# Kernel tuning notes

Measured on AMD Instinct MI355X. Metric: run time of the kernel, lower is better.

The kernel has to match this reference:

```python
import jax, jax.numpy as jnp
import numpy as np

BS, NCAMS, CIN, H, W = 4, 1, 256, 56, 200
MID = 128
DCH = 112  # (58-2)/0.5 depth bins
GX, GY, GZ = 128, 128, 16  # voxel grid


def setup_inputs() -> dict:
    key = jax.random.key(0)
    ks = jax.random.split(key, 32)
    f32 = jnp.float32

    def n(k, shape, scale=0.05):
        return jax.random.normal(k, shape, f32) * scale

    inp = {
        'img_feat': jax.random.normal(ks[0], (BS, NCAMS, CIN, H, W), f32),
        'scaled_pixel_size': jax.random.uniform(ks[1], (BS * NCAMS, 1), f32) * 2.0 + 0.5,
        # normalized sampling coords, slightly beyond [-1,1] to exercise zero padding
        'grids': jax.random.uniform(ks[2], (NCAMS, BS, GX, GY, GZ, 3), f32) * 2.2 - 1.1,
        # reduce_conv: Conv2d(CIN->MID,3x3,bias) + BN(affine, eval=per-channel scale/shift)
        'rc_w': n(ks[3], (MID, CIN, 3, 3)),
        'rc_b': n(ks[4], (MID,)),
        'rc_s': 1.0 + n(ks[5], (MID,)),
        'rc_t': n(ks[6], (MID,)),
        # Mlp(1 -> MID -> MID)
        'fc1_w': n(ks[7], (MID, 1), 0.5),
        'fc1_b': n(ks[8], (MID,)),
        'fc2_w': n(ks[9], (MID, MID)),
        'fc2_b': n(ks[10], (MID,)),
        # SELayer 1x1 convs (act on [N,MID,1,1] -> plain linears)
        'se_rw': n(ks[11], (MID, MID)),
        'se_rb': n(ks[12], (MID,)),
        'se_ew': n(ks[13], (MID, MID)),
        'se_eb': n(ks[14], (MID,)),
        # 3 BasicBlocks: conv3x3(no bias)+BN+ReLU+conv3x3(no bias)+BN, residual, ReLU
        'bb_w1': n(ks[15], (3, MID, MID, 3, 3)),
        'bb_s1': 1.0 + n(ks[16], (3, MID)),
        'bb_t1': n(ks[17], (3, MID)),
        'bb_w2': n(ks[18], (3, MID, MID, 3, 3)),
        'bb_s2': 1.0 + n(ks[19], (3, MID)),
        'bb_t2': n(ks[20], (3, MID)),
        # depth_pred 1x1 conv MID -> DCH
        'dp_w': n(ks[21], (DCH, MID)),
        'dp_b': n(ks[22], (DCH,)),
    }
    return inp


def _conv2d(x, w):
    return jax.lax.conv_general_dilated(x, w, (1, 1), 'SAME',
                                        dimension_numbers=('NCHW', 'OIHW', 'NCHW'))


def _aff(x, s, t):
    return x * s[None, :, None, None] + t[None, :, None, None]


def grid_sample_3d(feat, grid):
    """Trilinear grid_sample, zeros padding, align_corners=False.
    feat: [N,C,D,H,W]; grid: [N,X,Y,Z,3] with (x,y,z) in [-1,1] indexing (W,H,D).
    Returns [N,C,X,Y,Z]."""
    N, C, D, Hh, Ww = feat.shape
    ix = (grid[..., 0] + 1.0) * (Ww * 0.5) - 0.5
    iy = (grid[..., 1] + 1.0) * (Hh * 0.5) - 0.5
    iz = (grid[..., 2] + 1.0) * (D * 0.5) - 0.5
    x0 = jnp.floor(ix); y0 = jnp.floor(iy); z0 = jnp.floor(iz)
    fx, fy, fz = ix - x0, iy - y0, iz - z0

    def one(f, x0, y0, z0, fx, fy, fz):
        out = jnp.zeros((C,) + x0.shape, f.dtype)
        x0i = x0.astype(jnp.int32); y0i = y0.astype(jnp.int32); z0i = z0.astype(jnp.int32)
        for dz in (0, 1):
            for dy in (0, 1):
                for dx in (0, 1):
                    xi = x0i + dx; yi = y0i + dy; zi = z0i + dz
                    wgt = ((fx if dx else 1.0 - fx) * (fy if dy else 1.0 - fy)
                           * (fz if dz else 1.0 - fz))
                    valid = ((xi >= 0) & (xi < Ww) & (yi >= 0) & (yi < Hh)
                             & (zi >= 0) & (zi < D))
                    v = f[:, jnp.clip(zi, 0, D - 1), jnp.clip(yi, 0, Hh - 1),
                          jnp.clip(xi, 0, Ww - 1)]
                    out = out + v * (wgt * valid)[None]
        return out

    return jax.vmap(one)(feat, x0, y0, z0, fx, fy, fz)


def reference(img_feat, scaled_pixel_size, grids, rc_w, rc_b, rc_s, rc_t,
              fc1_w, fc1_b, fc2_w, fc2_b, se_rw, se_rb, se_ew, se_eb,
              bb_w1, bb_s1, bb_t1, bb_w2, bb_s2, bb_t2, dp_w, dp_b):
    bs, n_cams, c, h, w = img_feat.shape
    x = img_feat.reshape(bs * n_cams, c, h, w)
    # DepthNet (infer_mode): reduce_conv
    x = jax.nn.relu(_aff(_conv2d(x, rc_w) + rc_b[None, :, None, None], rc_s, rc_t))
    # Mlp on scaled_pixel_size + SE gating
    hmid = jax.nn.relu(scaled_pixel_size @ fc1_w.T + fc1_b) @ fc2_w.T + fc2_b
    se = jax.nn.relu(hmid @ se_rw.T + se_rb) @ se_ew.T + se_eb
    x = x * jax.nn.sigmoid(se)[:, :, None, None]
    # 3 BasicBlocks
    for i in range(3):
        y = jax.nn.relu(_aff(_conv2d(x, bb_w1[i]), bb_s1[i], bb_t1[i]))
        y = _aff(_conv2d(y, bb_w2[i]), bb_s2[i], bb_t2[i])
        x = jax.nn.relu(x + y)
    # depth_pred 1x1 conv, softmax over depth bins
    depth_feat = jnp.einsum('nchw,dc->ndhw', x, dp_w) + dp_b[None, :, None, None]
    depth = jax.nn.softmax(depth_feat, axis=1)
    depth = depth.reshape(bs, n_cams, 1, DCH, h, w)
    # per-camera frustum -> voxel bilinear sampling
    all_voxel_features = []
    for i in range(n_cams):
        all_voxel_features.append(grid_sample_3d(depth[:, i], grids[i]))
    agg = all_voxel_features[0]  # n_cams == 1 path in original forward
    return agg  # [bs, 1, GX, GY, GZ]
```

## Files before the change

### kernel.cpp

```cpp
#include <hip/hip_runtime.h>
#include <math.h>

typedef _Float16 v8h __attribute__((ext_vector_type(8)));
typedef float v4f __attribute__((ext_vector_type(4)));
typedef float v16f __attribute__((ext_vector_type(16)));

__global__ void __launch_bounds__(256) prep_kernel(
    const float* __restrict__ rc_w, const float* __restrict__ bb_w1,
    const float* __restrict__ bb_w2, const float* __restrict__ dp_w,
    const float* __restrict__ img, const float* __restrict__ sps,
    const float* __restrict__ fc1_w, const float* __restrict__ fc1_b,
    const float* __restrict__ fc2_w, const float* __restrict__ fc2_b,
    const float* __restrict__ se_rw, const float* __restrict__ se_rb,
    const float* __restrict__ se_ew, const float* __restrict__ se_eb,
    _Float16* __restrict__ wrc, _Float16* __restrict__ wbb,
    _Float16* __restrict__ wdp, _Float16* __restrict__ act16,
    float* __restrict__ sig) {
  const int bx = blockIdx.x;
  const int tid = threadIdx.x;
  __shared__ float lds[9224];

  if (bx < 32) {
    const float* src = rc_w + (size_t)bx * 4 * 2304;
#pragma unroll
    for (int r = 0; r < 36; ++r) {
      int e = r * 256 + tid;
      int col = e / 2304;
      int rem = e - col * 2304;
      lds[col * 2305 + rem] = src[e];
    }
    __syncthreads();
#pragma unroll
    for (int ro = 0; ro < 5; ++ro) {
      int lidx = ro * 256 + tid;
      if (lidx < 1152) {
        int col = lidx & 3;
        int r = lidx >> 2;
        int kh = r & 1;
        int ct = r >> 1;
        int tap = ct % 9, c16 = ct / 9;
        v8h o;
#pragma unroll
        for (int j = 0; j < 8; ++j)
          o[j] = (_Float16)lds[col * 2305 + (c16 * 16 + kh * 8 + j) * 9 + tap];
        *(v8h*)(wrc + ((size_t)r * 128 + bx * 4 + col) * 8) = o;
      }
    }
  } else if (bx < 128) {
    const int t = bx - 32;
    const int k = t >> 4, g = t & 15;
    const float* base = (k < 3) ? (bb_w1 + (size_t)k * 147456)
                                : (bb_w2 + (size_t)(k - 3) * 147456);
    const int cslot = (k < 3) ? (2 * k) : (2 * (k - 3) + 1);
    const float* src = base + (size_t)g * 8 * 1152;
#pragma unroll
    for (int r = 0; r < 36; ++r) {
      int e = r * 256 + tid;
      int col = e / 1152;
      int rem = e - col * 1152;
      lds[col * 1153 + rem] = src[e];
    }
    __syncthreads();
#pragma unroll
    for (int ro = 0; ro < 5; ++ro) {
      int lidx = ro * 256 + tid;
      if (lidx < 1152) {
        int col = lidx & 7;
        int r = lidx >> 3;
        int kh = r & 1;
        int ct = r >> 1;
        int tap = ct % 9, c16 = ct / 9;
        v8h o;
#pragma unroll
        for (int j = 0; j < 8; ++j)
          o[j] = (_Float16)lds[col * 1153 + (c16 * 16 + kh * 8 + j) * 9 + tap];
        *(v8h*)(wbb + (size_t)cslot * 147456 + ((size_t)r * 128 + g * 8 + col) * 8) = o;
      }
    }
  } else if (bx < 135) {
    int s3 = (bx - 128) * 256 + tid;
    v8h o;
#pragma unroll
    for (int j = 0; j < 8; ++j) o[j] = (_Float16)dp_w[(size_t)s3 * 8 + j];
    *(v8h*)(wdp + (size_t)s3 * 8) = o;
  } else if (bx == 135) {
    const int j = tid;
    const bool on = j < 128;
    for (int b = 0; b < 4; ++b) {
      float h1 = 0.f;
      if (on) h1 = fmaxf(sps[b] * fc1_w[j] + fc1_b[j], 0.f);
      __syncthreads();
      if (on) lds[j] = h1;
      __syncthreads();
      float hm = 0.f;
      if (on) {
        hm = fc2_b[j];
        for (int k = 0; k < 128; ++k) hm += lds[k] * fc2_w[j * 128 + k];
      }
      __syncthreads();
      if (on) lds[j] = hm;
      __syncthreads();
      float t = 0.f;
      if (on) {
        t = se_rb[j];
        for (int k = 0; k < 128; ++k) t += lds[k] * se_rw[j * 128 + k];
        t = fmaxf(t, 0.f);
      }
      __syncthreads();
      if (on) lds[j] = t;
      __syncthreads();
      if (on) {
        float se = se_eb[j];
        for (int k = 0; k < 128; ++k) se += lds[k] * se_ew[j * 128 + k];
        sig[b * 128 + j] = 1.f / (1.f + expf(-se));
      }
      __syncthreads();
    }
  } else {
    const int bid = bx - 136;
    const int n = bid / 56, h = bid - n * 56;
    const int w = tid;
    if (w < 200) {
      const float* ip = img + ((size_t)n * 256 * 56 + h) * 200 + w;
      _Float16* op = act16 + (((size_t)n * 56 + h) * 200 + w) * 256;
#pragma unroll 4
      for (int c8 = 0; c8 < 32; ++c8) {
        v8h o;
#pragma unroll
        for (int j = 0; j < 8; ++j)
          o[j] = (_Float16)ip[(size_t)(c8 * 8 + j) * 11200];
        *(v8h*)(op + c8 * 8) = o;
      }
    }
  }
}

template <int CIN, int MODE>
__global__ void __launch_bounds__(256, 4) conv3x3_kernel(
    const _Float16* __restrict__ act, const _Float16* __restrict__ wr,
    const _Float16* __restrict__ xprev, const float* __restrict__ bias,
    const float* __restrict__ sc, const float* __restrict__ tr,
    const float* __restrict__ sig_se, _Float16* __restrict__ out) {
  constexpr int NCH = CIN / 16;
  const int wt = blockIdx.x, ht = blockIdx.y;
  const int n = blockIdx.z >> 2, cq = blockIdx.z & 3;
  const int h0 = ht * 8, w0 = wt * 32;
  const int tid = threadIdx.x;
  const int wave = tid >> 6, lane = tid & 63;
  const int l31 = lane & 31, khalf = lane >> 5;
  const int wv = wave;

  __shared__ alignas(16) _Float16 ldsA[2][2 * 340 * 8];
  __shared__ alignas(16) _Float16 ldsB[2][576 * 8];

  size_t goffA[3];
  int loffA[3];
  bool exA[3], okA[3];
#pragma unroll
  for (int it = 0; it < 3; ++it) {
    int slot = it * 256 + tid;
    int pos = slot >> 1, part = slot & 1;
    int hh = pos / 34, ww = pos - hh * 34;
    int gh = h0 - 1 + hh, gw = w0 - 1 + ww;
    exA[it] = slot < 680;
    bool inimg = (unsigned)gh < 56u && (unsigned)gw < 200u;
    okA[it] = exA[it] && inimg;
    loffA[it] = (part * 340 + pos) * 8;
    int ghc = okA[it] ? gh : 0, gwc = okA[it] ? gw : 0;
    goffA[it] = (((size_t)n * 56 + ghc) * 200 + gwc) * CIN + part * 8;
  }
  size_t goffB[3];
  int loffB[3];
  bool exB[3];
#pragma unroll
  for (int it = 0; it < 3; ++it) {
    int slot = it * 256 + tid;
    exB[it] = slot < 576;
    int s = exB[it] ? slot : 0;
    int tap = s >> 6, kh = (s >> 5) & 1, co = s & 31;
    goffB[it] = (((size_t)(tap * 2 + kh)) * 128 + cq * 32 + co) * 8;
    loffB[it] = s * 8;
  }

  const v8h zero8 = {(_Float16)0, (_Float16)0, (_Float16)0, (_Float16)0,
                     (_Float16)0, (_Float16)0, (_Float16)0, (_Float16)0};
  v8h preA[3], preB[3];
#pragma unroll
  for (int it = 0; it < 3; ++it) preA[it] = okA[it] ? *(const v8h*)(act + goffA[it]) : zero8;
#pragma unroll
  for (int it = 0; it < 3; ++it) preB[it] = exB[it] ? *(const v8h*)(wr + goffB[it]) : zero8;

  v16f acc[2];
#pragma unroll
  for (int mt = 0; mt < 2; ++mt)
#pragma unroll
    for (int r = 0; r < 16; ++r) acc[mt][r] = 0.f;

#pragma unroll 1
  for (int c = 0; c < NCH; ++c) {
    _Float16* aB = &ldsA[c & 1][0];
    _Float16* bB = &ldsB[c & 1][0];
#pragma unroll
    for (int it = 0; it < 3; ++it)
      if (exA[it]) *(v8h*)(aB + loffA[it]) = preA[it];
#pragma unroll
    for (int it = 0; it < 3; ++it)
      if (exB[it]) *(v8h*)(bB + loffB[it]) = preB[it];
    __syncthreads();
    if (c + 1 < NCH) {
#pragma unroll
      for (int it = 0; it < 3; ++it)
        preA[it] = okA[it] ? *(const v8h*)(act + goffA[it] + (size_t)(c + 1) * 16) : zero8;
#pragma unroll
      for (int it = 0; it < 3; ++it)
        preB[it] = exB[it] ? *(const v8h*)(wr + goffB[it] + (size_t)(c + 1) * 18432) : zero8;
    }
#pragma unroll
    for (int dy = 0; dy < 3; ++dy) {
#pragma unroll
      for (int dx = 0; dx < 3; ++dx) {
        const int tap = dy * 3 + dx;
        v8h bfrag = *(const v8h*)(bB + (tap * 64 + khalf * 32 + l31) * 8);
#pragma unroll
        for (int mt = 0; mt < 2; ++mt) {
          const int pos = (wv * 2 + mt + dy) * 34 + l31 + dx;
          v8h afrag = *(const v8h*)(aB + (khalf * 340 + pos) * 8);
          acc[mt] = __builtin_amdgcn_mfma_f32_32x32x16_f16(afrag, bfrag, acc[mt], 0, 0, 0);
        }
      }
    }
  }

#pragma unroll
  for (int mt = 0; mt < 2; ++mt) {
    const int h = h0 + wv * 2 + mt;
    const int cc = cq * 32 + l31;
    const float s = sc[cc], t = tr[cc];
    float bb = 0.f, sg = 1.f;
    if constexpr (MODE == 0) {
      bb = bias[cc];
      sg = sig_se[n * 128 + cc];
    }
#pragma unroll
    for (int r = 0; r < 16; ++r) {
      const int m = (r & 3) + 8 * (r >> 2) + 4 * khalf;
      const int w = w0 + m;
      if (w < 200) {
        float v = acc[mt][r];
        size_t oidx = (((size_t)n * 56 + h) * 200 + w) * 128 + cc;
        if constexpr (MODE == 0) v = fmaxf((v + bb) * s + t, 0.f) * sg;
        if constexpr (MODE == 1) v = fmaxf(v * s + t, 0.f);
        if constexpr (MODE == 2) v = fmaxf((float)xprev[oidx] + v * s + t, 0.f);
        out[oidx] = (_Float16)v;
      }
    }
  }
}

__global__ void __launch_bounds__(256) depth_proj_softmax_kernel(
    const _Float16* __restrict__ x, const _Float16* __restrict__ wdp,
    const float* __restrict__ dp_b, _Float16* __restrict__ depth) {
  const int wave = threadIdx.x >> 6, lane = threadIdx.x & 63;
  const int q = lane >> 4, l16 = lane & 15;
  const int pos0 = blockIdx.x * 64 + wave * 16;

  v4f acc[7];
#pragma unroll
  for (int nt = 0; nt < 7; ++nt) {
    float bv = dp_b[nt * 16 + l16];
    acc[nt] = {bv, bv, bv, bv};
  }
#pragma unroll
  for (int c0 = 0; c0 < 128; c0 += 32) {
    v8h a = *(const v8h*)(x + (size_t)(pos0 + l16) * 128 + c0 + q * 8);
#pragma unroll
    for (int nt = 0; nt < 7; ++nt) {
      v8h b = *(const v8h*)(wdp + (size_t)(nt * 16 + l16) * 128 + c0 + q * 8);
      acc[nt] = __builtin_amdgcn_mfma_f32_16x16x32_f16(a, b, acc[nt], 0, 0, 0);
    }
  }
  float m[4];
#pragma unroll
  for (int r = 0; r < 4; ++r) {
    m[r] = acc[0][r];
#pragma unroll
    for (int nt = 1; nt < 7; ++nt) m[r] = fmaxf(m[r], acc[nt][r]);
  }
#pragma unroll
  for (int off = 1; off < 16; off <<= 1)
#pragma unroll
    for (int r = 0; r < 4; ++r) m[r] = fmaxf(m[r], __shfl_xor(m[r], off));
  float s[4] = {0.f, 0.f, 0.f, 0.f};
#pragma unroll
  for (int nt = 0; nt < 7; ++nt)
#pragma unroll
    for (int r = 0; r < 4; ++r) {
      float e = expf(acc[nt][r] - m[r]);
      acc[nt][r] = e;
      s[r] += e;
    }
#pragma unroll
  for (int off = 1; off < 16; off <<= 1)
#pragma unroll
    for (int r = 0; r < 4; ++r) s[r] += __shfl_xor(s[r], off);
#pragma unroll
  for (int r = 0; r < 4; ++r) {
    const float inv = 1.f / s[r];
    const size_t p = pos0 + q * 4 + r;
#pragma unroll
    for (int nt = 0; nt < 7; ++nt)
      depth[p * 112 + nt * 16 + l16] = (_Float16)(acc[nt][r] * inv);
  }
}

__global__ void __launch_bounds__(256) gridsample_kernel(
    const float* __restrict__ grids, const _Float16* __restrict__ depth,
    float* __restrict__ out) {
  const int i = blockIdx.x * 256 + threadIdx.x;
  const int n = i >> 18;
  const float gx = grids[(size_t)i * 3];
  const float gy = grids[(size_t)i * 3 + 1];
  const float gz = grids[(size_t)i * 3 + 2];
  const float ix = (gx + 1.f) * 100.f - 0.5f;
  const float iy = (gy + 1.f) * 28.f - 0.5f;
  const float iz = (gz + 1.f) * 56.f - 0.5f;
  const float xf = floorf(ix), yf = floorf(iy), zf = floorf(iz);
  const int x0 = (int)xf, y0 = (int)yf, z0 = (int)zf;
  const float fx = ix - xf, fy = iy - yf, fz = iz - zf;
  const bool zv0 = (unsigned)z0 < 112u;
  const bool zv1 = (unsigned)(z0 + 1) < 112u;
  const float wz0 = 1.f - fz, wz1 = fz;
  float acc = 0.f;
#pragma unroll
  for (int dy = 0; dy < 2; ++dy) {
    const int yi = y0 + dy;
    const float wy = dy ? fy : 1.f - fy;
#pragma unroll
    for (int dx = 0; dx < 2; ++dx) {
      const int xi = x0 + dx;
      const float wx = dx ? fx : 1.f - fx;
      if ((unsigned)xi < 200u && (unsigned)yi < 56u) {
        const _Float16* bp = depth + ((size_t)n * 11200 + yi * 200 + xi) * 112;
        float v0 = zv0 ? (float)bp[z0] : 0.f;
        float v1 = zv1 ? (float)bp[z0 + 1] : 0.f;
        acc += (wx * wy) * (wz0 * v0 + wz1 * v1);
      }
    }
  }
  out[i] = acc;
}

extern "C" void kernel_launch(void* const* d_in, const int* in_sizes, int n_in,
                              void* d_out, int out_size, void* d_ws, size_t ws_size,
                              hipStream_t stream) {
  (void)in_sizes; (void)n_in; (void)out_size; (void)ws_size;
  const float* img = (const float*)d_in[0];
  const float* sps = (const float*)d_in[1];
  const float* grids = (const float*)d_in[2];
  const float* rc_w = (const float*)d_in[3];
  const float* rc_b = (const float*)d_in[4];
  const float* rc_s = (const float*)d_in[5];
  const float* rc_t = (const float*)d_in[6];
  const float* fc1_w = (const float*)d_in[7];
  const float* fc1_b = (const float*)d_in[8];
  const float* fc2_w = (const float*)d_in[9];
  const float* fc2_b = (const float*)d_in[10];
  const float* se_rw = (const float*)d_in[11];
  const float* se_rb = (const float*)d_in[12];
  const float* se_ew = (const float*)d_in[13];
  const float* se_eb = (const float*)d_in[14];
  const float* bb_w1 = (const float*)d_in[15];
  const float* bb_s1 = (const float*)d_in[16];
  const float* bb_t1 = (const float*)d_in[17];
  const float* bb_w2 = (const float*)d_in[18];
  const float* bb_s2 = (const float*)d_in[19];
  const float* bb_t2 = (const float*)d_in[20];
  const float* dp_w = (const float*)d_in[21];
  const float* dp_b = (const float*)d_in[22];
  float* outp = (float*)d_out;

  char* ws = (char*)d_ws;
  _Float16* act16 = (_Float16*)(ws + 0);
  _Float16* depth16 = (_Float16*)(ws + 0);
  _Float16* xa = (_Float16*)(ws + 23068672);
  _Float16* xb = (_Float16*)(ws + 23068672 + 11534336);
  _Float16* yb = (_Float16*)(ws + 23068672 + 2 * 11534336);
  _Float16* wrc = (_Float16*)(ws + 57671680);
  _Float16* wdp = (_Float16*)(ws + 57671680 + 589824);
  _Float16* wbb = (_Float16*)(ws + 58327040);
  float* sig = (float*)(ws + 58327040 + 1769472);

  prep_kernel<<<dim3(360), 256, 0, stream>>>(
      rc_w, bb_w1, bb_w2, dp_w, img, sps, fc1_w, fc1_b, fc2_w, fc2_b, se_rw, se_rb,
      se_ew, se_eb, wrc, wbb, wdp, act16, sig);

  dim3 cgrid(7, 7, 16);
  conv3x3_kernel<256, 0><<<cgrid, 256, 0, stream>>>(act16, wrc, nullptr, rc_b, rc_s,
                                                    rc_t, sig, xa);
  _Float16* xcur = xa;
  _Float16* xnxt = xb;
  for (int i = 0; i < 3; ++i) {
    conv3x3_kernel<128, 1><<<cgrid, 256, 0, stream>>>(
        xcur, wbb + (size_t)(2 * i) * 147456, nullptr, nullptr, bb_s1 + i * 128,
        bb_t1 + i * 128, nullptr, yb);
    conv3x3_kernel<128, 2><<<cgrid, 256, 0, stream>>>(
        yb, wbb + (size_t)(2 * i + 1) * 147456, xcur, nullptr, bb_s2 + i * 128,
        bb_t2 + i * 128, nullptr, xnxt);
    _Float16* t = xcur;
    xcur = xnxt;
    xnxt = t;
  }

  depth_proj_softmax_kernel<<<dim3(700), 256, 0, stream>>>(xcur, wdp, dp_b, depth16);
  gridsample_kernel<<<dim3(4096), 256, 0, stream>>>(grids, depth16, outp);
}
```

Measured before the change: 418.6 us.

## Load conv weights directly into registers and reuse A fragments across dy taps

The conv3x3 kernel no longer stages weight tiles through LDS. Each lane now loads its nine B fragments for the current channel chunk straight from global memory into registers. The inner loop is reordered to iterate dx outermost, loading four rows of A fragments once and reusing them across the three dy taps. This cuts LDS traffic and removes the separate ldsB buffer. In exchange, global weight loads are no longer prefetched a chunk ahead and now sit on the critical path before each barrier, and register pressure rises under launch bounds of 4 blocks per CU.

New measurement: 446.9 us. +6.8%, slower.

```diff
diff --git a/kernel.cpp b/kernel.cpp
--- a/kernel.cpp
+++ b/kernel.cpp
@@ -151,7 +151,6 @@
   const int wv = wave;
 
   __shared__ alignas(16) _Float16 ldsA[2][2 * 340 * 8];
-  __shared__ alignas(16) _Float16 ldsB[2][576 * 8];
 
   size_t goffA[3];
   int loffA[3];
@@ -169,26 +168,13 @@
     int ghc = okA[it] ? gh : 0, gwc = okA[it] ? gw : 0;
     goffA[it] = (((size_t)n * 56 + ghc) * 200 + gwc) * CIN + part * 8;
   }
-  size_t goffB[3];
-  int loffB[3];
-  bool exB[3];
-#pragma unroll
-  for (int it = 0; it < 3; ++it) {
-    int slot = it * 256 + tid;
-    exB[it] = slot < 576;
-    int s = exB[it] ? slot : 0;
-    int tap = s >> 6, kh = (s >> 5) & 1, co = s & 31;
-    goffB[it] = (((size_t)(tap * 2 + kh)) * 128 + cq * 32 + co) * 8;
-    loffB[it] = s * 8;
-  }
+  const _Float16* wbase = wr + ((size_t)khalf * 128 + cq * 32 + l31) * 8;
 
   const v8h zero8 = {(_Float16)0, (_Float16)0, (_Float16)0, (_Float16)0,
                      (_Float16)0, (_Float16)0, (_Float16)0, (_Float16)0};
-  v8h preA[3], preB[3];
+  v8h preA[3];
 #pragma unroll
   for (int it = 0; it < 3; ++it) preA[it] = okA[it] ? *(const v8h*)(act + goffA[it]) : zero8;
-#pragma unroll
-  for (int it = 0; it < 3; ++it) preB[it] = exB[it] ? *(const v8h*)(wr + goffB[it]) : zero8;
 
   v16f acc[2];
 #pragma unroll
@@ -199,34 +185,30 @@
 #pragma unroll 1
   for (int c = 0; c < NCH; ++c) {
     _Float16* aB = &ldsA[c & 1][0];
-    _Float16* bB = &ldsB[c & 1][0];
 #pragma unroll
     for (int it = 0; it < 3; ++it)
       if (exA[it]) *(v8h*)(aB + loffA[it]) = preA[it];
-#pragma unroll
-    for (int it = 0; it < 3; ++it)
-      if (exB[it]) *(v8h*)(bB + loffB[it]) = preB[it];
+    v8h bfr[9];
+#pragma unroll
+    for (int tap = 0; tap < 9; ++tap)
+      bfr[tap] = *(const v8h*)(wbase + ((size_t)c * 2304 + tap * 256) * 8);
     __syncthreads();
     if (c + 1 < NCH) {
 #pragma unroll
       for (int it = 0; it < 3; ++it)
         preA[it] = okA[it] ? *(const v8h*)(act + goffA[it] + (size_t)(c + 1) * 16) : zero8;
-#pragma unroll
-      for (int it = 0; it < 3; ++it)
-        preB[it] = exB[it] ? *(const v8h*)(wr + goffB[it] + (size_t)(c + 1) * 18432) : zero8;
-    }
-#pragma unroll
-    for (int dy = 0; dy < 3; ++dy) {
-#pragma unroll
-      for (int dx = 0; dx < 3; ++dx) {
-        const int tap = dy * 3 + dx;
-        v8h bfrag = *(const v8h*)(bB + (tap * 64 + khalf * 32 + l31) * 8);
-#pragma unroll
-        for (int mt = 0; mt < 2; ++mt) {
-          const int pos = (wv * 2 + mt + dy) * 34 + l31 + dx;
-          v8h afrag = *(const v8h*)(aB + (khalf * 340 + pos) * 8);
-          acc[mt] = __builtin_amdgcn_mfma_f32_32x32x16_f16(afrag, bfrag, acc[mt], 0, 0, 0);
-        }
+    }
+#pragma unroll
+    for (int dx = 0; dx < 3; ++dx) {
+      v8h a[4];
+#pragma unroll
+      for (int r = 0; r < 4; ++r)
+        a[r] = *(const v8h*)(aB + (khalf * 340 + (wv * 2 + r) * 34 + l31 + dx) * 8);
+#pragma unroll
+      for (int dy = 0; dy < 3; ++dy) {
+        const v8h bf = bfr[dy * 3 + dx];
+        acc[0] = __builtin_amdgcn_mfma_f32_32x32x16_f16(a[dy], bf, acc[0], 0, 0, 0);
+        acc[1] = __builtin_amdgcn_mfma_f32_32x32x16_f16(a[dy + 1], bf, acc[1], 0, 0, 0);
       }
     }
   }
```
